# Kernel tuning notes

Hardware: AMD Instinct MI355X
Metric: run time of the kernel (lower is better)

Reference implementation:

```python
import jax, jax.numpy as jnp
import numpy as np
import math

B, S, D, H = 4, 2048, 1024, 16
DK = D // H


def setup_inputs() -> dict:
    key = jax.random.key(0)
    k1, k2, k3, k4, k5 = jax.random.split(key, 5)
    inputs = jax.random.normal(k1, (B, S, D), dtype=jnp.float32)
    # additive causal mask: 0 on/below diagonal, -1e9 above
    causal = jnp.triu(jnp.full((S, S), -1e9, dtype=jnp.float32), k=1)
    mask = causal[None, None, :, :]  # [1,1,S,S]
    w_qkv = jax.random.normal(k2, (D, 3 * D), dtype=jnp.float32) * 0.02
    b_qkv = jax.random.normal(k3, (3 * D,), dtype=jnp.float32) * 0.02
    w_head = jax.random.normal(k4, (D, D), dtype=jnp.float32) * 0.02
    b_head = jax.random.normal(k5, (D,), dtype=jnp.float32) * 0.02
    return {"inputs": inputs, "mask": mask, "w_qkv": w_qkv, "b_qkv": b_qkv,
            "w_head": w_head, "b_head": b_head}


def reference(inputs, mask, w_qkv, b_qkv, w_head, b_head):
    # fused QKV projection
    qkv = jnp.einsum('bsd,de->bse', inputs, w_qkv) + b_qkv  # [B,S,3D]
    q, k, v = jnp.split(qkv, 3, axis=-1)
    # split heads -> [B,H,S,DK]
    q = q.reshape(B, S, H, DK).transpose(0, 2, 1, 3)
    k = k.reshape(B, S, H, DK).transpose(0, 2, 1, 3)
    v = v.reshape(B, S, H, DK).transpose(0, 2, 1, 3)
    # scaled dot-product attention with additive mask
    att = jnp.einsum('bhqd,bhkd->bhqk', q, k) / math.sqrt(DK)
    att = att + mask
    att = jax.nn.softmax(att, axis=-1)  # dropout p=0 -> identity
    out = jnp.einsum('bhqk,bhkd->bhqd', att, v)  # [B,H,S,DK]
    # merge heads
    out = out.transpose(0, 2, 1, 3).reshape(B, S, D)
    out = jnp.einsum('bsd,de->bse', out, w_head) + b_head
    return out
```

## Files before the change

kernel.cpp:

```cpp
#include <hip/hip_runtime.h>
#include <stdint.h>

typedef __bf16 bf16x8 __attribute__((ext_vector_type(8)));
typedef __bf16 bf16x4 __attribute__((ext_vector_type(4)));
typedef float f32x4 __attribute__((ext_vector_type(4)));
typedef unsigned short u16;

__device__ __forceinline__ u16 f2bf(float f) {
  union { float f; unsigned u; } v; v.f = f;
  return (u16)((v.u + 0x7fffu + ((v.u >> 16) & 1u)) >> 16);
}

#define GLOAD_LDS16(gp, lp)                                                       \
  __builtin_amdgcn_global_load_lds((__attribute__((address_space(1))) void*)(gp), \
                                   (__attribute__((address_space(3))) void*)(lp), \
                                   16, 0, 0)

__global__ void k_cvt_bf16(const float* __restrict__ in, u16* __restrict__ out, int n4) {
  int i = blockIdx.x * blockDim.x + threadIdx.x;
  if (i >= n4) return;
  float4 v = ((const float4*)in)[i];
  ushort4 o;
  o.x = f2bf(v.x); o.y = f2bf(v.y); o.z = f2bf(v.z); o.w = f2bf(v.w);
  ((ushort4*)out)[i] = o;
}

__global__ void k_transpose_bf16(const float* __restrict__ w, u16* __restrict__ wt,
                                 int K, int N) {
  __shared__ u16 t[32][33];
  int n0 = blockIdx.x * 32, k0 = blockIdx.y * 32;
  int tx = threadIdx.x & 31, ty = threadIdx.x >> 5;
#pragma unroll
  for (int j = 0; j < 4; ++j) {
    int r = ty + j * 8;
    t[r][tx] = f2bf(w[(size_t)(k0 + r) * N + n0 + tx]);
  }
  __syncthreads();
#pragma unroll
  for (int j = 0; j < 4; ++j) {
    int r = ty + j * 8;
    wt[(size_t)(n0 + r) * K + k0 + tx] = t[tx][r];
  }
}

template <int MODE>
__global__ void __launch_bounds__(256, 2)
k_gemm_bt(const u16* __restrict__ A, const u16* __restrict__ Bt,
          const float* __restrict__ bias, u16* __restrict__ outQ,
          u16* __restrict__ outK, u16* __restrict__ outVt,
          float* __restrict__ outF, int Kdim, int Ncols) {
  __shared__ u16 Asq[128 * 64];
  __shared__ u16 Bsq[128 * 64];
  const int tid = threadIdx.x;
  const int lane = tid & 63;
  const int wv = tid >> 6;
  const int g = lane >> 4;
  const int lr = lane & 15;
  const int wr = wv >> 1, wc = wv & 1;
  const int row0 = blockIdx.y * 128;
  const int col0 = blockIdx.x * 128;

  const f32x4 fzero = {0.f, 0.f, 0.f, 0.f};
  f32x4 acc[4][4];
#pragma unroll
  for (int m = 0; m < 4; ++m)
#pragma unroll
    for (int n = 0; n < 4; ++n) acc[m][n] = fzero;

  const u16* Arow = A + (size_t)row0 * Kdim;
  const u16* Brow = Bt + (size_t)col0 * Kdim;

  for (int kt = 0; kt < Kdim; kt += 64) {
#pragma unroll
    for (int j = 0; j < 4; ++j) {
      int unit = j * 256 + wv * 64 + lane;
      int r = unit >> 3, u = unit & 7;
      int ug = u ^ (r & 7);
      GLOAD_LDS16(Arow + (size_t)r * Kdim + kt + ug * 8,
                  &Asq[(size_t)(j * 256 + wv * 64) * 8]);
      GLOAD_LDS16(Brow + (size_t)r * Kdim + kt + ug * 8,
                  &Bsq[(size_t)(j * 256 + wv * 64) * 8]);
    }
    __syncthreads();
#pragma unroll
    for (int kc = 0; kc < 2; ++kc) {
      bf16x8 af[4], bfr[4];
#pragma unroll
      for (int m = 0; m < 4; ++m) {
        int r = wr * 64 + m * 16 + lr;
        int u = (kc * 4 + g) ^ (r & 7);
        af[m] = *(const bf16x8*)((const char*)Asq + r * 128 + u * 16);
      }
#pragma unroll
      for (int n = 0; n < 4; ++n) {
        int r = wc * 64 + n * 16 + lr;
        int u = (kc * 4 + g) ^ (r & 7);
        bfr[n] = *(const bf16x8*)((const char*)Bsq + r * 128 + u * 16);
      }
#pragma unroll
      for (int m = 0; m < 4; ++m)
#pragma unroll
        for (int n = 0; n < 4; ++n)
          acc[m][n] = __builtin_amdgcn_mfma_f32_16x16x32_bf16(af[m], bfr[n],
                                                              acc[m][n], 0, 0, 0);
    }
    __syncthreads();
  }

#pragma unroll
  for (int n = 0; n < 4; ++n) {
    int e = col0 + wc * 64 + n * 16 + lr;
    float bv = bias[e];
    if (MODE == 0) {
      int part = e >> 10;
      int d = e & 1023;
      int hh = d >> 6;
      int dk = d & 63;
#pragma unroll
      for (int m = 0; m < 4; ++m) {
        int tbase = row0 + wr * 64 + m * 16 + g * 4;
        int bb = tbase >> 11;
        int s = tbase & 2047;
        size_t bh = (size_t)((bb << 4) + hh);
        if (part == 2) {
          ushort4 pk;
          pk.x = f2bf(acc[m][n][0] + bv);
          pk.y = f2bf(acc[m][n][1] + bv);
          pk.z = f2bf(acc[m][n][2] + bv);
          pk.w = f2bf(acc[m][n][3] + bv);
          *(ushort4*)(outVt + (bh * 64 + dk) * 2048 + s) = pk;
        } else {
#pragma unroll
          for (int i = 0; i < 4; ++i) {
            float val = acc[m][n][i] + bv;
            size_t off = (bh * 2048 + (size_t)(s + i)) * 64 + dk;
            if (part == 0)
              outQ[off] = f2bf(val * 0.125f);
            else
              outK[off] = f2bf(val);
          }
        }
      }
    } else {
#pragma unroll
      for (int m = 0; m < 4; ++m)
#pragma unroll
        for (int i = 0; i < 4; ++i) {
          int t = row0 + wr * 64 + m * 16 + g * 4 + i;
          outF[(size_t)t * Ncols + e] = acc[m][n][i] + bv;
        }
    }
  }
}


__device__ __forceinline__ void stage_kv(const u16* __restrict__ Kb,
                                         const u16* __restrict__ Vb, int kbase,
                                         u16* Kbuf, u16* Vbuf, int wv, int lane) {
#pragma unroll
  for (int j = 0; j < 2; ++j) {
    int unit = j * 256 + wv * 64 + lane;
    int r = unit >> 3, u = unit & 7;
    int ug = u ^ (r & 7);
    GLOAD_LDS16(Kb + (size_t)(kbase + r) * 64 + ug * 8, Kbuf + (j * 256 + wv * 64) * 8);
    GLOAD_LDS16(Vb + (size_t)r * 2048 + kbase + ug * 8, Vbuf + (j * 256 + wv * 64) * 8);
  }
}

__device__ __forceinline__ void attn_tile(const u16* Kbuf, const u16* Vbuf, u16* Pw,
                                          const bf16x8* qf, f32x4* o, float& mrow,
                                          float& lrow, int q0, int kbase, int lr,
                                          int g) {
  const f32x4 fzero = {0.f, 0.f, 0.f, 0.f};
  f32x4 s[4];
  __builtin_amdgcn_s_setprio(1);
#pragma unroll
  for (int cf = 0; cf < 4; ++cf) {
    s[cf] = fzero;
#pragma unroll
    for (int kc = 0; kc < 2; ++kc) {
      int r = cf * 16 + lr;
      int us = (kc * 4 + g) ^ (r & 7);
      bf16x8 kf = *(const bf16x8*)(Kbuf + r * 64 + us * 8);
      s[cf] = __builtin_amdgcn_mfma_f32_16x16x32_bf16(kf, qf[kc], s[cf], 0, 0, 0);
    }
  }
  __builtin_amdgcn_s_setprio(0);
  const int q = q0 + lr;
  if (kbase + 63 > q0) {
#pragma unroll
    for (int cf = 0; cf < 4; ++cf)
#pragma unroll
      for (int i = 0; i < 4; ++i)
        if (kbase + cf * 16 + 4 * g + i > q) s[cf][i] = -1e30f;
  }
  float tm = -1e30f;
#pragma unroll
  for (int cf = 0; cf < 4; ++cf)
#pragma unroll
    for (int i = 0; i < 4; ++i) tm = fmaxf(tm, s[cf][i]);
  tm = fmaxf(tm, __shfl_xor(tm, 16));
  tm = fmaxf(tm, __shfl_xor(tm, 32));
  if (__all(tm - mrow <= 8.f)) {
    float rs = 0.f;
#pragma unroll
    for (int cf = 0; cf < 4; ++cf)
#pragma unroll
      for (int i = 0; i < 4; ++i) {
        s[cf][i] = __expf(s[cf][i] - mrow);
        rs += s[cf][i];
      }
    rs += __shfl_xor(rs, 16);
    rs += __shfl_xor(rs, 32);
    lrow += rs;
  } else {
    float mn = fmaxf(mrow, tm);
    float alpha = __expf(mrow - mn);
    mrow = mn;
    float rs = 0.f;
#pragma unroll
    for (int cf = 0; cf < 4; ++cf)
#pragma unroll
      for (int i = 0; i < 4; ++i) {
        s[cf][i] = __expf(s[cf][i] - mn);
        rs += s[cf][i];
      }
    rs += __shfl_xor(rs, 16);
    rs += __shfl_xor(rs, 32);
    lrow = lrow * alpha + rs;
#pragma unroll
    for (int cf = 0; cf < 4; ++cf)
#pragma unroll
      for (int i = 0; i < 4; ++i) o[cf][i] *= alpha;
  }
#pragma unroll
  for (int cf = 0; cf < 4; ++cf) {
    bf16x4 ph;
    ph[0] = (__bf16)s[cf][0];
    ph[1] = (__bf16)s[cf][1];
    ph[2] = (__bf16)s[cf][2];
    ph[3] = (__bf16)s[cf][3];
    int uw = (2 * cf + (g >> 1)) ^ (lr & 7);
    *(bf16x4*)(Pw + lr * 64 + uw * 8 + (g & 1) * 4) = ph;
  }
  __builtin_amdgcn_s_setprio(1);
#pragma unroll
  for (int kc = 0; kc < 2; ++kc) {
    int ur = (4 * kc + g) ^ (lr & 7);
    bf16x8 pb = *(const bf16x8*)(Pw + lr * 64 + ur * 8);
#pragma unroll
    for (int cf = 0; cf < 4; ++cf) {
      int r = cf * 16 + lr;
      int us = (kc * 4 + g) ^ (r & 7);
      bf16x8 vf = *(const bf16x8*)(Vbuf + r * 64 + us * 8);
      o[cf] = __builtin_amdgcn_mfma_f32_16x16x32_bf16(vf, pb, o[cf], 0, 0, 0);
    }
  }
  __builtin_amdgcn_s_setprio(0);
}

__global__ void __launch_bounds__(256, 4)
k_flash(const u16* __restrict__ Qg, const u16* __restrict__ Kg,
        const u16* __restrict__ Vtg, u16* __restrict__ attn) {
  __shared__ u16 KV[2][2][4096];
  __shared__ u16 P_lds[4][16][64];
  const int tid = threadIdx.x;
  const int lane = tid & 63;
  const int wv = tid >> 6;
  const int g = lane >> 4;
  const int lr = lane & 15;

  const int flat = blockIdx.x;
  const int swz = (flat & 7) * 128 + (flat >> 3);
  const int qa_t = swz & 15;
  const int qb_t = 31 - qa_t;
  const int bh = swz >> 4;

  const u16* Qb = Qg + (size_t)bh * 2048 * 64;
  const u16* Kb = Kg + (size_t)bh * 2048 * 64;
  const u16* Vb = Vtg + (size_t)bh * 64 * 2048;
  u16* Pw = &P_lds[wv][0][0];

  const int q0a = qa_t * 64 + wv * 16;
  const int q0b = qb_t * 64 + wv * 16;

  bf16x8 qfa[2], qfb[2];
#pragma unroll
  for (int kc = 0; kc < 2; ++kc) {
    qfa[kc] = *(const bf16x8*)(Qb + (size_t)(q0a + lr) * 64 + kc * 32 + g * 8);
    qfb[kc] = *(const bf16x8*)(Qb + (size_t)(q0b + lr) * 64 + kc * 32 + g * 8);
  }

  const f32x4 fzero = {0.f, 0.f, 0.f, 0.f};
  f32x4 oa[4], ob[4];
#pragma unroll
  for (int cf = 0; cf < 4; ++cf) { oa[cf] = fzero; ob[cf] = fzero; }
  float mra = -1e30f, lra = 0.f, mrb = -1e30f, lrb = 0.f;

  stage_kv(Kb, Vb, 0, &KV[0][0][0], &KV[0][1][0], wv, lane);
  __syncthreads();

  for (int kt = 0; kt <= qb_t; ++kt) {
    const int nb = kt & 1;
    const u16* Kbuf = &KV[nb][0][0];
    const u16* Vbuf = &KV[nb][1][0];
    if (kt < qb_t)
      stage_kv(Kb, Vb, (kt + 1) * 64, &KV[nb ^ 1][0][0], &KV[nb ^ 1][1][0], wv, lane);
    attn_tile(Kbuf, Vbuf, Pw, qfb, ob, mrb, lrb, q0b, kt * 64, lr, g);
    if (kt <= qa_t)
      attn_tile(Kbuf, Vbuf, Pw, qfa, oa, mra, lra, q0a, kt * 64, lr, g);
    __syncthreads();
  }

  const int bb = bh >> 4, hh = bh & 15;
  const float inv_a = 1.f / lra, inv_b = 1.f / lrb;
#pragma unroll
  for (int cf = 0; cf < 4; ++cf) {
    ushort4 pa, pb;
    pa.x = f2bf(oa[cf][0] * inv_a); pa.y = f2bf(oa[cf][1] * inv_a);
    pa.z = f2bf(oa[cf][2] * inv_a); pa.w = f2bf(oa[cf][3] * inv_a);
    pb.x = f2bf(ob[cf][0] * inv_b); pb.y = f2bf(ob[cf][1] * inv_b);
    pb.z = f2bf(ob[cf][2] * inv_b); pb.w = f2bf(ob[cf][3] * inv_b);
    size_t dcol = hh * 64 + cf * 16 + 4 * g;
    *(ushort4*)(attn + ((size_t)(bb * 2048 + q0a + lr)) * 1024 + dcol) = pa;
    *(ushort4*)(attn + ((size_t)(bb * 2048 + q0b + lr)) * 1024 + dcol) = pb;
  }
}

extern "C" void kernel_launch(void* const* d_in, const int* in_sizes, int n_in,
                              void* d_out, int out_size, void* d_ws, size_t ws_size,
                              hipStream_t stream) {
  const float* x      = (const float*)d_in[0];
  const float* w_qkv  = (const float*)d_in[2];
  const float* b_qkv  = (const float*)d_in[3];
  const float* w_head = (const float*)d_in[4];
  const float* b_head = (const float*)d_in[5];
  float* out = (float*)d_out;

  u16* Xb    = (u16*)d_ws;
  u16* Wqkvt = Xb + (size_t)8192 * 1024;
  u16* Wht   = Wqkvt + (size_t)3072 * 1024;
  u16* Qw    = Wht + (size_t)1024 * 1024;
  u16* Kw    = Qw + (size_t)64 * 2048 * 64;
  u16* Vtw   = Kw + (size_t)64 * 2048 * 64;
  u16* Attn  = Xb;

  k_cvt_bf16<<<8192, 256, 0, stream>>>(x, Xb, (8192 * 1024) / 4);
  k_transpose_bf16<<<dim3(96, 32), 256, 0, stream>>>(w_qkv, Wqkvt, 1024, 3072);
  k_transpose_bf16<<<dim3(32, 32), 256, 0, stream>>>(w_head, Wht, 1024, 1024);
  k_gemm_bt<0><<<dim3(24, 64), 256, 0, stream>>>(Xb, Wqkvt, b_qkv, Qw, Kw, Vtw,
                                                 nullptr, 1024, 3072);
  k_flash<<<1024, 256, 0, stream>>>(Qw, Kw, Vtw, Attn);
  k_gemm_bt<1><<<dim3(8, 64), 256, 0, stream>>>(Attn, Wht, b_head, nullptr, nullptr,
                                                nullptr, out, 1024, 1024);
}
```

Baseline: 164.4 us.

## Rewrite flash attention with 32x32 MFMA tiles, register P exchange, exp2 softmax

Rewrites the flash-attention kernel so each wave handles 32 query rows with 32x32x16 bf16 MFMAs instead of 16-row 16x16x32 tiles. The P matrix is handed to the PV MFMA through cross-lane shuffles rather than an LDS round trip. Softmax now uses exp2, with log2(e) folded into the Q scale, and keeps the lazy-rescale threshold. The grid is halved to 512 blocks, each processing two 128-row query blocks sequentially for causal balance. This trades more registers per wave and less parallelism for fewer LDS accesses and denser matrix instructions.

```diff
diff --git a/kernel.cpp b/kernel.cpp
--- a/kernel.cpp
+++ b/kernel.cpp
@@ -2,13 +2,32 @@
 #include <stdint.h>
 
 typedef __bf16 bf16x8 __attribute__((ext_vector_type(8)));
-typedef __bf16 bf16x4 __attribute__((ext_vector_type(4)));
 typedef float f32x4 __attribute__((ext_vector_type(4)));
+typedef float f32x16 __attribute__((ext_vector_type(16)));
 typedef unsigned short u16;
+
+#if __has_builtin(__builtin_amdgcn_exp2f)
+#define EXP2F(x) __builtin_amdgcn_exp2f(x)
+#else
+#define EXP2F(x) exp2f(x)
+#endif
 
 __device__ __forceinline__ u16 f2bf(float f) {
   union { float f; unsigned u; } v; v.f = f;
   return (u16)((v.u + 0x7fffu + ((v.u >> 16) & 1u)) >> 16);
+}
+
+__device__ __forceinline__ unsigned pk2bf(float a, float b) {
+  union { __bf16 h[2]; unsigned u; } c;
+  c.h[0] = (__bf16)a; c.h[1] = (__bf16)b;
+  return c.u;
+}
+
+__device__ __forceinline__ f32x16 vz16() {
+  f32x16 v;
+#pragma unroll
+  for (int i = 0; i < 16; ++i) v[i] = 0.f;
+  return v;
 }
 
 #define GLOAD_LDS16(gp, lp)                                                       \
@@ -135,7 +154,7 @@
             float val = acc[m][n][i] + bv;
             size_t off = (bh * 2048 + (size_t)(s + i)) * 64 + dk;
             if (part == 0)
-              outQ[off] = f2bf(val * 0.125f);
+              outQ[off] = f2bf(val * 0.18033688f);
             else
               outK[off] = f2bf(val);
           }
@@ -167,163 +186,177 @@
   }
 }
 
-__device__ __forceinline__ void attn_tile(const u16* Kbuf, const u16* Vbuf, u16* Pw,
-                                          const bf16x8* qf, f32x4* o, float& mrow,
-                                          float& lrow, int q0, int kbase, int lr,
-                                          int g) {
-  const f32x4 fzero = {0.f, 0.f, 0.f, 0.f};
-  f32x4 s[4];
-  __builtin_amdgcn_s_setprio(1);
-#pragma unroll
-  for (int cf = 0; cf < 4; ++cf) {
-    s[cf] = fzero;
-#pragma unroll
-    for (int kc = 0; kc < 2; ++kc) {
-      int r = cf * 16 + lr;
-      int us = (kc * 4 + g) ^ (r & 7);
-      bf16x8 kf = *(const bf16x8*)(Kbuf + r * 64 + us * 8);
-      s[cf] = __builtin_amdgcn_mfma_f32_16x16x32_bf16(kf, qf[kc], s[cf], 0, 0, 0);
-    }
-  }
-  __builtin_amdgcn_s_setprio(0);
-  const int q = q0 + lr;
-  if (kbase + 63 > q0) {
-#pragma unroll
-    for (int cf = 0; cf < 4; ++cf)
-#pragma unroll
-      for (int i = 0; i < 4; ++i)
-        if (kbase + cf * 16 + 4 * g + i > q) s[cf][i] = -1e30f;
-  }
-  float tm = -1e30f;
-#pragma unroll
-  for (int cf = 0; cf < 4; ++cf)
-#pragma unroll
-    for (int i = 0; i < 4; ++i) tm = fmaxf(tm, s[cf][i]);
-  tm = fmaxf(tm, __shfl_xor(tm, 16));
-  tm = fmaxf(tm, __shfl_xor(tm, 32));
-  if (__all(tm - mrow <= 8.f)) {
-    float rs = 0.f;
-#pragma unroll
-    for (int cf = 0; cf < 4; ++cf)
-#pragma unroll
-      for (int i = 0; i < 4; ++i) {
-        s[cf][i] = __expf(s[cf][i] - mrow);
-        rs += s[cf][i];
-      }
-    rs += __shfl_xor(rs, 16);
-    rs += __shfl_xor(rs, 32);
-    lrow += rs;
-  } else {
-    float mn = fmaxf(mrow, tm);
-    float alpha = __expf(mrow - mn);
-    mrow = mn;
-    float rs = 0.f;
-#pragma unroll
-    for (int cf = 0; cf < 4; ++cf)
-#pragma unroll
-      for (int i = 0; i < 4; ++i) {
-        s[cf][i] = __expf(s[cf][i] - mn);
-        rs += s[cf][i];
-      }
-    rs += __shfl_xor(rs, 16);
-    rs += __shfl_xor(rs, 32);
-    lrow = lrow * alpha + rs;
-#pragma unroll
-    for (int cf = 0; cf < 4; ++cf)
-#pragma unroll
-      for (int i = 0; i < 4; ++i) o[cf][i] *= alpha;
-  }
-#pragma unroll
-  for (int cf = 0; cf < 4; ++cf) {
-    bf16x4 ph;
-    ph[0] = (__bf16)s[cf][0];
-    ph[1] = (__bf16)s[cf][1];
-    ph[2] = (__bf16)s[cf][2];
-    ph[3] = (__bf16)s[cf][3];
-    int uw = (2 * cf + (g >> 1)) ^ (lr & 7);
-    *(bf16x4*)(Pw + lr * 64 + uw * 8 + (g & 1) * 4) = ph;
-  }
-  __builtin_amdgcn_s_setprio(1);
-#pragma unroll
-  for (int kc = 0; kc < 2; ++kc) {
-    int ur = (4 * kc + g) ^ (lr & 7);
-    bf16x8 pb = *(const bf16x8*)(Pw + lr * 64 + ur * 8);
-#pragma unroll
-    for (int cf = 0; cf < 4; ++cf) {
-      int r = cf * 16 + lr;
-      int us = (kc * 4 + g) ^ (r & 7);
-      bf16x8 vf = *(const bf16x8*)(Vbuf + r * 64 + us * 8);
-      o[cf] = __builtin_amdgcn_mfma_f32_16x16x32_bf16(vf, pb, o[cf], 0, 0, 0);
-    }
-  }
-  __builtin_amdgcn_s_setprio(0);
-}
-
 __global__ void __launch_bounds__(256, 4)
 k_flash(const u16* __restrict__ Qg, const u16* __restrict__ Kg,
         const u16* __restrict__ Vtg, u16* __restrict__ attn) {
   __shared__ u16 KV[2][2][4096];
-  __shared__ u16 P_lds[4][16][64];
   const int tid = threadIdx.x;
   const int lane = tid & 63;
   const int wv = tid >> 6;
-  const int g = lane >> 4;
-  const int lr = lane & 15;
-
-  const int flat = blockIdx.x;
-  const int swz = (flat & 7) * 128 + (flat >> 3);
-  const int qa_t = swz & 15;
-  const int qb_t = 31 - qa_t;
-  const int bh = swz >> 4;
+  const int ql = lane & 31;
+  const int hi = lane >> 5;
+
+  const int bid = blockIdx.x;
+  const int pr = bid >> 6;
+  const int bh = bid & 63;
 
   const u16* Qb = Qg + (size_t)bh * 2048 * 64;
   const u16* Kb = Kg + (size_t)bh * 2048 * 64;
   const u16* Vb = Vtg + (size_t)bh * 64 * 2048;
-  u16* Pw = &P_lds[wv][0][0];
-
-  const int q0a = qa_t * 64 + wv * 16;
-  const int q0b = qb_t * 64 + wv * 16;
-
-  bf16x8 qfa[2], qfb[2];
-#pragma unroll
-  for (int kc = 0; kc < 2; ++kc) {
-    qfa[kc] = *(const bf16x8*)(Qb + (size_t)(q0a + lr) * 64 + kc * 32 + g * 8);
-    qfb[kc] = *(const bf16x8*)(Qb + (size_t)(q0b + lr) * 64 + kc * 32 + g * 8);
-  }
-
-  const f32x4 fzero = {0.f, 0.f, 0.f, 0.f};
-  f32x4 oa[4], ob[4];
-#pragma unroll
-  for (int cf = 0; cf < 4; ++cf) { oa[cf] = fzero; ob[cf] = fzero; }
-  float mra = -1e30f, lra = 0.f, mrb = -1e30f, lrb = 0.f;
-
-  stage_kv(Kb, Vb, 0, &KV[0][0][0], &KV[0][1][0], wv, lane);
-  __syncthreads();
-
-  for (int kt = 0; kt <= qb_t; ++kt) {
-    const int nb = kt & 1;
-    const u16* Kbuf = &KV[nb][0][0];
-    const u16* Vbuf = &KV[nb][1][0];
-    if (kt < qb_t)
-      stage_kv(Kb, Vb, (kt + 1) * 64, &KV[nb ^ 1][0][0], &KV[nb ^ 1][1][0], wv, lane);
-    attn_tile(Kbuf, Vbuf, Pw, qfb, ob, mrb, lrb, q0b, kt * 64, lr, g);
-    if (kt <= qa_t)
-      attn_tile(Kbuf, Vbuf, Pw, qfa, oa, mra, lra, q0a, kt * 64, lr, g);
+  const int bb = bh >> 4, hh = bh & 15;
+
+  int off[4];
+#pragma unroll
+  for (int j = 0; j < 4; ++j) off[j] = ql * 64 + (((2 * j + hi) ^ (ql & 7)) * 8);
+
+  for (int side = 0; side < 2; ++side) {
+    const int qb = side ? (15 - pr) : pr;
+    const int ntile = 2 * qb + 2;
+    const int q0w = qb * 128 + wv * 32;
+    const int q = q0w + ql;
+
+    bf16x8 qf[4];
+#pragma unroll
+    for (int ds = 0; ds < 4; ++ds)
+      qf[ds] = *(const bf16x8*)(Qb + (size_t)q * 64 + ds * 16 + hi * 8);
+
+    f32x16 o0 = vz16(), o1 = vz16();
+    float mrow = -1e30f, lrow = 0.f;
+
+    stage_kv(Kb, Vb, 0, &KV[0][0][0], &KV[0][1][0], wv, lane);
     __syncthreads();
-  }
-
-  const int bb = bh >> 4, hh = bh & 15;
-  const float inv_a = 1.f / lra, inv_b = 1.f / lrb;
-#pragma unroll
-  for (int cf = 0; cf < 4; ++cf) {
-    ushort4 pa, pb;
-    pa.x = f2bf(oa[cf][0] * inv_a); pa.y = f2bf(oa[cf][1] * inv_a);
-    pa.z = f2bf(oa[cf][2] * inv_a); pa.w = f2bf(oa[cf][3] * inv_a);
-    pb.x = f2bf(ob[cf][0] * inv_b); pb.y = f2bf(ob[cf][1] * inv_b);
-    pb.z = f2bf(ob[cf][2] * inv_b); pb.w = f2bf(ob[cf][3] * inv_b);
-    size_t dcol = hh * 64 + cf * 16 + 4 * g;
-    *(ushort4*)(attn + ((size_t)(bb * 2048 + q0a + lr)) * 1024 + dcol) = pa;
-    *(ushort4*)(attn + ((size_t)(bb * 2048 + q0b + lr)) * 1024 + dcol) = pb;
+
+    for (int kt = 0; kt < ntile; ++kt) {
+      const int kbase = kt * 64;
+      const int nb = kt & 1;
+      if (kt + 1 < ntile)
+        stage_kv(Kb, Vb, kbase + 64, &KV[nb ^ 1][0][0], &KV[nb ^ 1][1][0], wv, lane);
+      const u16* Kbuf = &KV[nb][0][0];
+      const u16* Vbuf = &KV[nb][1][0];
+
+      if (kbase <= q0w + 31) {
+        const bool need1 = (kbase + 32) <= (q0w + 31);
+        f32x16 s0 = vz16(), s1 = vz16();
+        __builtin_amdgcn_s_setprio(1);
+#pragma unroll
+        for (int ds = 0; ds < 4; ++ds) {
+          bf16x8 kf = *(const bf16x8*)(Kbuf + off[ds]);
+          s0 = __builtin_amdgcn_mfma_f32_32x32x16_bf16(kf, qf[ds], s0, 0, 0, 0);
+        }
+        if (need1) {
+#pragma unroll
+          for (int ds = 0; ds < 4; ++ds) {
+            bf16x8 kf = *(const bf16x8*)(Kbuf + 2048 + off[ds]);
+            s1 = __builtin_amdgcn_mfma_f32_32x32x16_bf16(kf, qf[ds], s1, 0, 0, 0);
+          }
+        }
+        __builtin_amdgcn_s_setprio(0);
+
+        if (kbase + 63 > q0w) {
+#pragma unroll
+          for (int r = 0; r < 16; ++r) {
+            const int krel = (r & 3) + 8 * (r >> 2) + 4 * hi;
+            if (kbase + krel > q) s0[r] = -1e30f;
+            if (kbase + 32 + krel > q) s1[r] = -1e30f;
+          }
+        }
+
+        float a0[8];
+#pragma unroll
+        for (int i = 0; i < 8; ++i)
+          a0[i] = fmaxf(fmaxf(s0[i], s0[i + 8]), fmaxf(s1[i], s1[i + 8]));
+        float a1[4];
+#pragma unroll
+        for (int i = 0; i < 4; ++i) a1[i] = fmaxf(a0[i], a0[i + 4]);
+        float tm = fmaxf(fmaxf(a1[0], a1[1]), fmaxf(a1[2], a1[3]));
+        tm = fmaxf(tm, __shfl_xor(tm, 32));
+
+        if (!__all(tm - mrow <= 11.5417f)) {
+          float mn = fmaxf(mrow, tm);
+          float al = EXP2F(mrow - mn);
+          mrow = mn;
+          lrow *= al;
+          o0 *= al;
+          o1 *= al;
+        }
+
+#pragma unroll
+        for (int r = 0; r < 16; ++r) {
+          s0[r] = EXP2F(s0[r] - mrow);
+          s1[r] = EXP2F(s1[r] - mrow);
+        }
+        float b0[8];
+#pragma unroll
+        for (int i = 0; i < 8; ++i)
+          b0[i] = (s0[i] + s0[i + 8]) + (s1[i] + s1[i + 8]);
+        float b1[4];
+#pragma unroll
+        for (int i = 0; i < 4; ++i) b1[i] = b0[i] + b0[i + 4];
+        float rs = (b1[0] + b1[1]) + (b1[2] + b1[3]);
+        rs += __shfl_xor(rs, 32);
+        lrow += rs;
+
+        unsigned W[4][4];
+#pragma unroll
+        for (int kc = 0; kc < 4; ++kc) {
+          if (kc < 2 || need1) {
+            const int h2 = kc & 1;
+            float v0 = (kc < 2) ? s0[8 * h2 + 0] : s1[8 * h2 + 0];
+            float v1 = (kc < 2) ? s0[8 * h2 + 1] : s1[8 * h2 + 1];
+            float v2 = (kc < 2) ? s0[8 * h2 + 2] : s1[8 * h2 + 2];
+            float v3 = (kc < 2) ? s0[8 * h2 + 3] : s1[8 * h2 + 3];
+            float v4 = (kc < 2) ? s0[8 * h2 + 4] : s1[8 * h2 + 4];
+            float v5 = (kc < 2) ? s0[8 * h2 + 5] : s1[8 * h2 + 5];
+            float v6 = (kc < 2) ? s0[8 * h2 + 6] : s1[8 * h2 + 6];
+            float v7 = (kc < 2) ? s0[8 * h2 + 7] : s1[8 * h2 + 7];
+            unsigned w0 = pk2bf(v0, v1), w1 = pk2bf(v2, v3);
+            unsigned w2 = pk2bf(v4, v5), w3 = pk2bf(v6, v7);
+            unsigned pw0 = (unsigned)__shfl_xor((int)w0, 32);
+            unsigned pw1 = (unsigned)__shfl_xor((int)w1, 32);
+            unsigned pw2 = (unsigned)__shfl_xor((int)w2, 32);
+            unsigned pw3 = (unsigned)__shfl_xor((int)w3, 32);
+            W[kc][0] = hi ? pw2 : w0;
+            W[kc][1] = hi ? pw3 : w1;
+            W[kc][2] = hi ? w2 : pw0;
+            W[kc][3] = hi ? w3 : pw1;
+          }
+        }
+
+        __builtin_amdgcn_s_setprio(1);
+#pragma unroll
+        for (int kc = 0; kc < 4; ++kc) {
+          if (kc < 2 || need1) {
+            union { unsigned u[4]; bf16x8 v; } pf;
+            pf.u[0] = W[kc][0]; pf.u[1] = W[kc][1];
+            pf.u[2] = W[kc][2]; pf.u[3] = W[kc][3];
+            bf16x8 vf0 = *(const bf16x8*)(Vbuf + off[kc]);
+            o0 = __builtin_amdgcn_mfma_f32_32x32x16_bf16(vf0, pf.v, o0, 0, 0, 0);
+            bf16x8 vf1 = *(const bf16x8*)(Vbuf + 2048 + off[kc]);
+            o1 = __builtin_amdgcn_mfma_f32_32x32x16_bf16(vf1, pf.v, o1, 0, 0, 0);
+          }
+        }
+        __builtin_amdgcn_s_setprio(0);
+      }
+      __syncthreads();
+    }
+
+    const float inv = 1.f / lrow;
+    const size_t rowoff = ((size_t)(bb * 2048 + q)) * 1024 + hh * 64;
+#pragma unroll
+    for (int r4 = 0; r4 < 4; ++r4) {
+      ushort4 pa;
+      pa.x = f2bf(o0[4 * r4 + 0] * inv);
+      pa.y = f2bf(o0[4 * r4 + 1] * inv);
+      pa.z = f2bf(o0[4 * r4 + 2] * inv);
+      pa.w = f2bf(o0[4 * r4 + 3] * inv);
+      *(ushort4*)(attn + rowoff + 8 * r4 + 4 * hi) = pa;
+      ushort4 pb;
+      pb.x = f2bf(o1[4 * r4 + 0] * inv);
+      pb.y = f2bf(o1[4 * r4 + 1] * inv);
+      pb.z = f2bf(o1[4 * r4 + 2] * inv);
+      pb.w = f2bf(o1[4 * r4 + 3] * inv);
+      *(ushort4*)(attn + rowoff + 32 + 8 * r4 + 4 * hi) = pb;
+    }
   }
 }
 
@@ -350,7 +383,7 @@
   k_transpose_bf16<<<dim3(32, 32), 256, 0, stream>>>(w_head, Wht, 1024, 1024);
   k_gemm_bt<0><<<dim3(24, 64), 256, 0, stream>>>(Xb, Wqkvt, b_qkv, Qw, Kw, Vtw,
                                                  nullptr, 1024, 3072);
-  k_flash<<<1024, 256, 0, stream>>>(Qw, Kw, Vtw, Attn);
+  k_flash<<<512, 256, 0, stream>>>(Qw, Kw, Vtw, Attn);
   k_gemm_bt<1><<<dim3(8, 64), 256, 0, stream>>>(Attn, Wht, b_head, nullptr, nullptr,
                                                 nullptr, out, 1024, 1024);
 }
```

Measured after the change: 170.9 us. +4.0%, slower.
